# Performance work log

Hardware: AMD Instinct MI355X
Metric: run time of the kernel (lower is better)

## Reference

```python
import jax, jax.numpy as jnp
import numpy as np

IMAGE_W = 640
IMAGE_H = 640
ALPHA = 0.25
GAMMA = 2.0
BETA = 1.0 / 9.0
EPS = 1e-4


def _make_anchors(image_w, image_h):
    # standard RetinaNet anchors: 3 ratios x 3 scales per location, 5 FPN levels
    strides = [8, 16, 32, 64, 128]
    base_sizes = [32, 64, 128, 256, 512]
    ratios = np.array([0.5, 1.0, 2.0])
    scales = np.array([2.0 ** 0, 2.0 ** (1.0 / 3.0), 2.0 ** (2.0 / 3.0)])
    all_boxes = []
    for s, b in zip(strides, base_sizes):
        fw, fh = image_w // s, image_h // s
        ws, hs = [], []
        for r in ratios:
            for sc in scales:
                area = (b * sc) ** 2
                w = np.sqrt(area / r)
                ws.append(w)
                hs.append(w * r)
        wh = np.stack([np.array(ws), np.array(hs)], axis=-1).reshape(1, -1, 2)
        cx = (np.arange(fw) + 0.5) * s
        cy = (np.arange(fh) + 0.5) * s
        cx, cy = np.meshgrid(cx, cy)
        ctr = np.stack([cx, cy], axis=-1).reshape(-1, 1, 2)
        boxes = np.concatenate([ctr - 0.5 * wh, ctr + 0.5 * wh], axis=-1).reshape(-1, 4)
        all_boxes.append(boxes)
    return np.concatenate(all_boxes, axis=0).astype(np.float32)  # [76725, 4]


def setup_inputs() -> dict:
    key = jax.random.key(0)
    k1, k2, k3, k4, k5 = jax.random.split(key, 5)
    B, C, M = 4, 80, 16
    anchors = jnp.asarray(_make_anchors(IMAGE_W, IMAGE_H))  # [N,4]
    N = anchors.shape[0]
    batch_anchors = jnp.broadcast_to(anchors[None], (B, N, 4))
    cls_heads = jax.random.uniform(k1, (B, N, C), minval=0.01, maxval=0.99, dtype=jnp.float32)
    reg_heads = jax.random.normal(k2, (B, N, 4), dtype=jnp.float32)
    xy = jax.random.uniform(k3, (B, M, 2), minval=0.0, maxval=480.0)
    wh = jax.random.uniform(k4, (B, M, 2), minval=32.0, maxval=160.0)
    boxes = jnp.concatenate([xy, jnp.minimum(xy + wh, 639.0)], axis=-1)
    labels = jax.random.randint(k5, (B, M), 0, C).astype(jnp.float32)
    valid = jnp.arange(M)[None, :] < 12  # last 4 gt slots are -1 padding
    annotations = jnp.where(valid[..., None],
                            jnp.concatenate([boxes, labels[..., None]], axis=-1),
                            -1.0)
    return {"cls_heads": cls_heads, "reg_heads": reg_heads,
            "batch_anchors": batch_anchors, "annotations": annotations}


def _assign_one_image(anchors, annots):
    # anchors [N,4], annots [M,5] (label<0 == padding)
    valid_gt = annots[:, 4] >= 0.0                                  # [M]
    boxes, cls = annots[:, :4], annots[:, 4]
    area_a = (anchors[:, 2] - anchors[:, 0]) * (anchors[:, 3] - anchors[:, 1])
    area_g = (boxes[:, 2] - boxes[:, 0]) * (boxes[:, 3] - boxes[:, 1])
    lt = jnp.maximum(anchors[:, None, :2], boxes[None, :, :2])      # [N,M,2]
    rb = jnp.minimum(anchors[:, None, 2:], boxes[None, :, 2:])
    wh = jnp.clip(rb - lt, 0.0)
    inter = wh[..., 0] * wh[..., 1]                                 # [N,M]
    iou = inter / (area_a[:, None] + area_g[None, :] - inter)
    iou = jnp.where(valid_gt[None, :], iou, -1.0)                   # ignore padded gts
    idx = jnp.argmax(iou, axis=1)                                   # [N]
    overlap = jnp.max(iou, axis=1)
    gt_box = boxes[idx]                                             # [N,4]
    gt_cls = cls[idx]
    # encode gt box as (tx,ty,tw,th) wrt anchor
    a_wh = anchors[:, 2:] - anchors[:, :2]
    a_ctr = anchors[:, :2] + 0.5 * a_wh
    g_wh = jnp.clip(gt_box[:, 2:] - gt_box[:, :2], 1.0)
    g_ctr = gt_box[:, :2] + 0.5 * g_wh
    targets = jnp.concatenate([(g_ctr - a_ctr) / a_wh, jnp.log(g_wh / a_wh)], axis=1)
    targets = targets / jnp.array([0.1, 0.1, 0.2, 0.2], dtype=targets.dtype)
    label = jnp.full_like(overlap, -1.0)
    label = jnp.where(overlap < 0.4, 0.0, label)
    label = jnp.where(overlap > 0.5, gt_cls + 1.0, label)
    label = jnp.where(jnp.any(valid_gt), label, -1.0)               # no gt -> all ignore
    return targets, label


def reference(cls_heads, reg_heads, batch_anchors, annotations):
    # mask (instead of filter) out-of-border anchors: equivalent to dropping them
    a = batch_anchors
    inside = (a[..., 0] > 0) & (a[..., 1] > 0) & (a[..., 2] < IMAGE_W) & (a[..., 3] < IMAGE_H)
    targets, labels = jax.vmap(_assign_one_image)(batch_anchors, annotations)  # [B,N,4],[B,N]
    labels = jnp.where(inside, labels, -1.0)

    cls_mask = labels >= 0.0          # anchors counted in focal loss
    pos_mask = labels > 0.0           # positive anchors
    pos = jnp.sum(pos_mask, axis=1).astype(cls_heads.dtype)  # [B]

    # focal (cls) loss
    p = jnp.clip(cls_heads, EPS, 1.0 - EPS)                   # [B,N,C]
    num_classes = cls_heads.shape[-1]
    gt_onehot = jax.nn.one_hot(labels.astype(jnp.int32), num_classes + 1,
                               dtype=cls_heads.dtype)[..., 1:]  # [B,N,C]
    is_pos = gt_onehot > 0.5
    alpha_f = jnp.where(is_pos, ALPHA, 1.0 - ALPHA)
    pt = jnp.where(is_pos, p, 1.0 - p)
    focal_w = alpha_f * (1.0 - pt) ** GAMMA
    bce = -gt_onehot * jnp.log(p) - (1.0 - gt_onehot) * jnp.log(1.0 - p)
    fl = focal_w * bce
    cls_per_img = jnp.sum(fl * cls_mask[..., None], axis=(1, 2)) / jnp.maximum(pos, 1.0)

    # smooth-L1 (reg) loss over positive anchors
    x = jnp.abs(reg_heads - targets)
    sl1 = jnp.where(x < BETA, 0.5 * x * x / BETA, x - 0.5 * BETA)
    reg_per_img = jnp.sum(sl1 * pos_mask[..., None], axis=(1, 2)) / jnp.maximum(4.0 * pos, 1.0)

    valid_img = pos > 0.0
    n_valid = jnp.maximum(jnp.sum(valid_img.astype(cls_heads.dtype)), 1.0)
    cls_loss = jnp.sum(jnp.where(valid_img, cls_per_img, 0.0)) / n_valid
    reg_loss = jnp.sum(jnp.where(valid_img, reg_per_img, 0.0)) / n_valid
    return (cls_loss, reg_loss)
```

## Files before the change

kernel.cpp:

```cpp
#include <hip/hip_runtime.h>
#include <cmath>

#define GT_CAP 64
#define NCH 20

typedef float fvec4 __attribute__((ext_vector_type(4)));

__global__ __launch_bounds__(256, 4) void retina_main(
    const float* __restrict__ cls_heads,
    const float* __restrict__ reg_heads,
    const float* __restrict__ anchors,
    const float* __restrict__ annots,
    float* __restrict__ ws,
    int N, int M, int B)
{
    const int b  = blockIdx.y;
    const int n0 = blockIdx.x << 8;
    const int t  = threadIdx.x;

    __shared__ float s_ann[5 * GT_CAP];
    __shared__ float s_lab[256];
    __shared__ float s_red[12];

    const int mm = (M > GT_CAP) ? GT_CAP : M;
    for (int i = t; i < 5 * mm; i += 256)
        s_ann[i] = annots[(size_t)b * 5 * M + i];
    __syncthreads();

    float reg_acc = 0.0f;
    float pos_cnt = 0.0f;
    float label   = -1.0f;
    const int n = n0 + t;
    if (n < N) {
        const float4 a = *(const float4*)(anchors + (size_t)n * 4);
        const bool inside = (a.x > 0.0f) && (a.y > 0.0f) &&
                            (a.z < 640.0f) && (a.w < 640.0f);
        if (inside) {
            const float area_a = (a.z - a.x) * (a.w - a.y);
            float best = -3.0e38f;
            int   bi   = 0;
            bool  any  = false;
            for (int m = 0; m < mm; ++m) {
                const float gx1 = s_ann[m*5+0], gy1 = s_ann[m*5+1];
                const float gx2 = s_ann[m*5+2], gy2 = s_ann[m*5+3];
                const float gc  = s_ann[m*5+4];
                float v = -1.0f;
                if (gc >= 0.0f) {
                    any = true;
                    const float iw = fmaxf(fminf(a.z, gx2) - fmaxf(a.x, gx1), 0.0f);
                    const float ih = fmaxf(fminf(a.w, gy2) - fmaxf(a.y, gy1), 0.0f);
                    const float inter = iw * ih;
                    v = inter / (area_a + (gx2 - gx1) * (gy2 - gy1) - inter);
                }
                if (v > best) { best = v; bi = m; }
            }
            if (any) {
                if (best < 0.4f)      label = 0.0f;
                else if (best > 0.5f) label = s_ann[bi*5+4] + 1.0f;
            }
            if (label > 0.0f) {
                pos_cnt = 1.0f;
                const float aw = a.z - a.x, ah = a.w - a.y;
                const float acx = a.x + 0.5f * aw, acy = a.y + 0.5f * ah;
                const float gw = fmaxf(s_ann[bi*5+2] - s_ann[bi*5+0], 1.0f);
                const float gh = fmaxf(s_ann[bi*5+3] - s_ann[bi*5+1], 1.0f);
                const float gcx = s_ann[bi*5+0] + 0.5f * gw;
                const float gcy = s_ann[bi*5+1] + 0.5f * gh;
                const float tx = (gcx - acx) / aw * 10.0f;
                const float ty = (gcy - acy) / ah * 10.0f;
                const float tw = __logf(gw / aw) * 5.0f;
                const float th = __logf(gh / ah) * 5.0f;
                const float4 r = *(const float4*)(reg_heads + ((size_t)b * N + n) * 4);
                const float dx[4] = { fabsf(r.x - tx), fabsf(r.y - ty),
                                      fabsf(r.z - tw), fabsf(r.w - th) };
                #pragma unroll
                for (int j = 0; j < 4; ++j) {
                    const float x = dx[j];
                    reg_acc += (x < (1.0f / 9.0f)) ? 4.5f * x * x
                                                   : x - (1.0f / 18.0f);
                }
            }
        }
    }
    s_lab[t] = label;
    const int anyValid = __syncthreads_or(label >= 0.0f ? 1 : 0);

    float cls_acc = 0.0f;
    if (anyValid) {
        const float* plane = cls_heads + (size_t)b * (size_t)N * 80;
        const unsigned base_off  = (unsigned)n0 * 80u + 4u * (unsigned)t;
        const unsigned plane_max = (unsigned)N * 80u - 4u;

        fvec4 pb[NCH];
        #pragma unroll
        for (int k = 0; k < NCH; ++k) {
            unsigned off = base_off + 1024u * (unsigned)k;
            off = (off > plane_max) ? plane_max : off;
            pb[k] = *(const fvec4*)(plane + off);
        }

        int ap = t / 20;
        int c4 = t - (t / 20) * 20;
        #pragma unroll
        for (int k = 0; k < NCH; ++k) {
            const float lab  = s_lab[ap];
            const fvec4 v    = pb[k];
            const float mask = (lab >= 0.0f) ? 1.0f : 0.0f;
            const float cb   = (float)(c4 * 4 + 1);
            float local = 0.0f;
            #pragma unroll
            for (int j = 0; j < 4; ++j) {
                const float p = fminf(fmaxf(v[j], 1.0e-4f), 1.0f - 1.0e-4f);
                const bool  is_pos = (lab == cb + (float)j);
                const float pt     = is_pos ? p : 1.0f - p;
                const float alpha  = is_pos ? 0.25f : 0.75f;
                const float om     = 1.0f - pt;
                local += alpha * om * om * (-__logf(pt));
            }
            cls_acc += mask * local;
            ap += 12; c4 += 16; if (c4 >= 20) { c4 -= 20; ++ap; }
        }
    }

    const int lane = t & 63, wid = t >> 6;
    #pragma unroll
    for (int off = 32; off > 0; off >>= 1) {
        cls_acc += __shfl_down(cls_acc, off, 64);
        reg_acc += __shfl_down(reg_acc, off, 64);
        pos_cnt += __shfl_down(pos_cnt, off, 64);
    }
    if (lane == 0) {
        s_red[wid]     = cls_acc;
        s_red[4 + wid] = reg_acc;
        s_red[8 + wid] = pos_cnt;
    }
    __syncthreads();
    if (t == 0) {
        const float c = s_red[0] + s_red[1] + s_red[2]  + s_red[3];
        const float r = s_red[4] + s_red[5] + s_red[6]  + s_red[7];
        const float p = s_red[8] + s_red[9] + s_red[10] + s_red[11];
        if (c != 0.0f) atomicAdd(&ws[b], c);
        if (r != 0.0f) atomicAdd(&ws[B + b], r);
        if (p != 0.0f) atomicAdd(&ws[2 * B + b], p);
    }
}

__global__ void retina_final(const float* __restrict__ ws,
                             float* __restrict__ out, int B)
{
    if (threadIdx.x == 0 && blockIdx.x == 0) {
        float cl = 0.0f, rl = 0.0f, nv = 0.0f;
        for (int b = 0; b < B; ++b) {
            const float pos = ws[2 * B + b];
            if (pos > 0.0f) {
                cl += ws[b]     / fmaxf(pos, 1.0f);
                rl += ws[B + b] / fmaxf(4.0f * pos, 1.0f);
                nv += 1.0f;
            }
        }
        const float n = fmaxf(nv, 1.0f);
        out[0] = cl / n;
        out[1] = rl / n;
    }
}

extern "C" void kernel_launch(void* const* d_in, const int* in_sizes, int n_in,
                              void* d_out, int out_size, void* d_ws, size_t ws_size,
                              hipStream_t stream) {
    const float* cls = (const float*)d_in[0];
    const float* reg = (const float*)d_in[1];
    const float* anc = (const float*)d_in[2];
    const float* ann = (const float*)d_in[3];

    const int B = 4;
    const int N = in_sizes[1] / (4 * B);
    const int M = in_sizes[3] / (5 * B);
    float* ws = (float*)d_ws;

    (void)hipMemsetAsync(d_ws, 0, 12 * sizeof(float), stream);

    dim3 grid((N + 255) / 256, B);
    retina_main<<<grid, 256, 0, stream>>>(cls, reg, anc, ann, ws, N, M, B);
    retina_final<<<1, 64, 0, stream>>>(ws, (float*)d_out, B);
}
```

Baseline: 172.2 us.

## Split fused kernel into anchor-assignment and grid-stride focal-loss kernels

The single fused kernel is split in two. The first kernel does the IoU assignment and the smooth-L1 loss and writes a per-anchor label byte to workspace. The second is a grid-stride kernel with a fixed 512x4 grid that streams the class scores as float4 quads, reads each label byte and accumulates the focal loss. This is meant to decouple the bandwidth-bound focal pass from the assignment work and its register pressure, at the cost of an extra launch and a round trip of the label array through global memory.

```diff
diff --git a/kernel.cpp b/kernel.cpp
--- a/kernel.cpp
+++ b/kernel.cpp
@@ -2,25 +2,23 @@
 #include <cmath>
 
 #define GT_CAP 64
-#define NCH 20
 
 typedef float fvec4 __attribute__((ext_vector_type(4)));
 
-__global__ __launch_bounds__(256, 4) void retina_main(
-    const float* __restrict__ cls_heads,
+__global__ __launch_bounds__(256) void retina_assign(
     const float* __restrict__ reg_heads,
     const float* __restrict__ anchors,
     const float* __restrict__ annots,
     float* __restrict__ ws,
+    unsigned char* __restrict__ lab8,
     int N, int M, int B)
 {
-    const int b  = blockIdx.y;
-    const int n0 = blockIdx.x << 8;
-    const int t  = threadIdx.x;
+    const int b = blockIdx.y;
+    const int n = (blockIdx.x << 8) + threadIdx.x;
+    const int t = threadIdx.x;
 
     __shared__ float s_ann[5 * GT_CAP];
-    __shared__ float s_lab[256];
-    __shared__ float s_red[12];
+    __shared__ float s_red[8];
 
     const int mm = (M > GT_CAP) ? GT_CAP : M;
     for (int i = t; i < 5 * mm; i += 256)
@@ -30,7 +28,6 @@
     float reg_acc = 0.0f;
     float pos_cnt = 0.0f;
     float label   = -1.0f;
-    const int n = n0 + t;
     if (n < N) {
         const float4 a = *(const float4*)(anchors + (size_t)n * 4);
         const bool inside = (a.x > 0.0f) && (a.y > 0.0f) &&
@@ -81,67 +78,80 @@
                 }
             }
         }
-    }
-    s_lab[t] = label;
-    const int anyValid = __syncthreads_or(label >= 0.0f ? 1 : 0);
-
-    float cls_acc = 0.0f;
-    if (anyValid) {
-        const float* plane = cls_heads + (size_t)b * (size_t)N * 80;
-        const unsigned base_off  = (unsigned)n0 * 80u + 4u * (unsigned)t;
-        const unsigned plane_max = (unsigned)N * 80u - 4u;
-
-        fvec4 pb[NCH];
-        #pragma unroll
-        for (int k = 0; k < NCH; ++k) {
-            unsigned off = base_off + 1024u * (unsigned)k;
-            off = (off > plane_max) ? plane_max : off;
-            pb[k] = *(const fvec4*)(plane + off);
-        }
-
-        int ap = t / 20;
-        int c4 = t - (t / 20) * 20;
-        #pragma unroll
-        for (int k = 0; k < NCH; ++k) {
-            const float lab  = s_lab[ap];
-            const fvec4 v    = pb[k];
-            const float mask = (lab >= 0.0f) ? 1.0f : 0.0f;
-            const float cb   = (float)(c4 * 4 + 1);
-            float local = 0.0f;
-            #pragma unroll
-            for (int j = 0; j < 4; ++j) {
-                const float p = fminf(fmaxf(v[j], 1.0e-4f), 1.0f - 1.0e-4f);
-                const bool  is_pos = (lab == cb + (float)j);
-                const float pt     = is_pos ? p : 1.0f - p;
-                const float alpha  = is_pos ? 0.25f : 0.75f;
-                const float om     = 1.0f - pt;
-                local += alpha * om * om * (-__logf(pt));
-            }
-            cls_acc += mask * local;
-            ap += 12; c4 += 16; if (c4 >= 20) { c4 -= 20; ++ap; }
-        }
+        lab8[(size_t)b * N + n] = (unsigned char)(label + 1.0f);
     }
 
     const int lane = t & 63, wid = t >> 6;
     #pragma unroll
     for (int off = 32; off > 0; off >>= 1) {
-        cls_acc += __shfl_down(cls_acc, off, 64);
         reg_acc += __shfl_down(reg_acc, off, 64);
         pos_cnt += __shfl_down(pos_cnt, off, 64);
     }
-    if (lane == 0) {
-        s_red[wid]     = cls_acc;
-        s_red[4 + wid] = reg_acc;
-        s_red[8 + wid] = pos_cnt;
-    }
+    if (lane == 0) { s_red[wid] = reg_acc; s_red[4 + wid] = pos_cnt; }
     __syncthreads();
     if (t == 0) {
-        const float c = s_red[0] + s_red[1] + s_red[2]  + s_red[3];
-        const float r = s_red[4] + s_red[5] + s_red[6]  + s_red[7];
-        const float p = s_red[8] + s_red[9] + s_red[10] + s_red[11];
-        if (c != 0.0f) atomicAdd(&ws[b], c);
+        const float r = s_red[0] + s_red[1] + s_red[2] + s_red[3];
+        const float p = s_red[4] + s_red[5] + s_red[6] + s_red[7];
         if (r != 0.0f) atomicAdd(&ws[B + b], r);
         if (p != 0.0f) atomicAdd(&ws[2 * B + b], p);
+    }
+}
+
+__device__ __forceinline__ float quad_loss(const float* __restrict__ plane,
+                                           const unsigned char* __restrict__ labp,
+                                           unsigned q)
+{
+    const unsigned a  = q / 20u;
+    const unsigned c4 = q - a * 20u;
+    const int   lv = (int)labp[a];
+    const fvec4 v  = *(const fvec4*)(plane + 4u * (size_t)q);
+    const int   cb = (int)(c4 * 4u) + 2;
+    float local = 0.0f;
+    #pragma unroll
+    for (int j = 0; j < 4; ++j) {
+        const float p      = fminf(fmaxf(v[j], 1.0e-4f), 1.0f - 1.0e-4f);
+        const bool  is_pos = (lv == cb + j);
+        const float pt     = is_pos ? p : 1.0f - p;
+        const float alpha  = is_pos ? 0.25f : 0.75f;
+        const float om     = 1.0f - pt;
+        local += alpha * om * om * (-__logf(pt));
+    }
+    return (lv >= 1) ? local : 0.0f;
+}
+
+__global__ __launch_bounds__(256) void retina_focal(
+    const float* __restrict__ cls_heads,
+    const unsigned char* __restrict__ lab8,
+    float* __restrict__ ws,
+    int N)
+{
+    const int b = blockIdx.y;
+    const int t = threadIdx.x;
+    const unsigned TOTP   = (unsigned)N * 20u;
+    const unsigned STRIDE = gridDim.x << 8;
+
+    const float*         plane = cls_heads + (size_t)b * (size_t)N * 80;
+    const unsigned char* labp  = lab8 + (size_t)b * (size_t)N;
+
+    __shared__ float s_red[4];
+
+    float acc = 0.0f;
+    unsigned q = (blockIdx.x << 8) + (unsigned)t;
+    for (; q + STRIDE < TOTP; q += 2u * STRIDE) {
+        acc += quad_loss(plane, labp, q);
+        acc += quad_loss(plane, labp, q + STRIDE);
+    }
+    if (q < TOTP) acc += quad_loss(plane, labp, q);
+
+    const int lane = t & 63, wid = t >> 6;
+    #pragma unroll
+    for (int off = 32; off > 0; off >>= 1)
+        acc += __shfl_down(acc, off, 64);
+    if (lane == 0) s_red[wid] = acc;
+    __syncthreads();
+    if (t == 0) {
+        const float c = s_red[0] + s_red[1] + s_red[2] + s_red[3];
+        if (c != 0.0f) atomicAdd(&ws[b], c);
     }
 }
 
@@ -176,10 +186,15 @@
     const int N = in_sizes[1] / (4 * B);
     const int M = in_sizes[3] / (5 * B);
     float* ws = (float*)d_ws;
+    unsigned char* lab8 = (unsigned char*)d_ws + 48;
 
     (void)hipMemsetAsync(d_ws, 0, 12 * sizeof(float), stream);
 
-    dim3 grid((N + 255) / 256, B);
-    retina_main<<<grid, 256, 0, stream>>>(cls, reg, anc, ann, ws, N, M, B);
+    dim3 gridA((N + 255) / 256, B);
+    retina_assign<<<gridA, 256, 0, stream>>>(reg, anc, ann, ws, lab8, N, M, B);
+
+    dim3 gridB(512, B);
+    retina_focal<<<gridB, 256, 0, stream>>>(cls, lab8, ws, N);
+
     retina_final<<<1, 64, 0, stream>>>(ws, (float*)d_out, B);
 }
```

Result: slower. 177.4 us (+3.0%).
